# Kernel optimization log

Measured on AMD Instinct MI355X. Metric: run time of the kernel, lower is better.

The kernel has to match this reference:

```python
import jax, jax.numpy as jnp
import numpy as np

N_NODES = 50000
N_EDGES = 800000
D = 128


def _gcn_norm(edge_index, edge_weights, n_nodes):
    # PyG gcn_norm with add_self_loops=True, fill_value=1.0
    src = jnp.concatenate([edge_index[0], jnp.arange(n_nodes)])
    dst = jnp.concatenate([edge_index[1], jnp.arange(n_nodes)])
    w = jnp.concatenate([edge_weights, jnp.ones((n_nodes,), edge_weights.dtype)])
    deg = jax.ops.segment_sum(w, dst, num_segments=n_nodes)
    dinv = jnp.where(deg > 0, jax.lax.rsqrt(deg), 0.0)
    norm = dinv[src] * w * dinv[dst]  # [E + N]
    return src, dst, norm


def _gcn_conv(x, src, dst, norm, W, b, n_nodes):
    h = x @ W                                   # [N, F_out]
    msg = h[src] * norm[:, None]                # gather + scale, [E+N, F_out]
    out = jax.ops.segment_sum(msg, dst, num_segments=n_nodes)
    return out + b


def setup_inputs() -> dict:
    key = jax.random.key(0)
    ks = jax.random.split(key, 12)
    s = 1.0 / np.sqrt(D)
    return {
        "x": jax.random.normal(ks[0], (N_NODES, D), jnp.float32),
        "edge_index": jax.random.randint(ks[1], (2, N_EDGES), 0, N_NODES, jnp.int64),
        "edge_weights": jax.random.uniform(ks[2], (N_EDGES,), jnp.float32),
        "W1": jax.random.normal(ks[3], (D, D), jnp.float32) * s,
        "b1": jnp.zeros((D,), jnp.float32),
        "W2": jax.random.normal(ks[4], (D, D), jnp.float32) * s,
        "b2": jnp.zeros((D,), jnp.float32),
        "W3": jax.random.normal(ks[5], (D, D), jnp.float32) * s,
        "b3": jnp.zeros((D,), jnp.float32),
        "Wl": jax.random.normal(ks[6], (D, D), jnp.float32) * s,
        "bl": jnp.zeros((D,), jnp.float32),
    }


def reference(x, edge_index, edge_weights, W1, b1, W2, b2, W3, b3, Wl, bl):
    n = x.shape[0]
    src, dst, norm = _gcn_norm(edge_index, edge_weights, n)
    h = _gcn_conv(x, src, dst, norm, W1, b1, n)
    h = jax.nn.relu(h)
    h = _gcn_conv(h, src, dst, norm, W2, b2, n)
    h = jax.nn.relu(h)
    h = _gcn_conv(h, src, dst, norm, W3, b3, n)
    # final 'linear' activation entry == nn.Linear(out_size, out_size)
    return h @ Wl + bl
```

## Files before the change

kernel.cpp:

```cpp
#include <hip/hip_runtime.h>
#include <hip/hip_fp16.h>


#define D 128

typedef __attribute__((ext_vector_type(8))) _Float16 half8;
typedef __attribute__((ext_vector_type(4))) float floatx4;

#define CNT_STRIDE 16

__global__ __launch_bounds__(256) void k_edge_pass1(const int* __restrict__ dst,
                                                    unsigned int* __restrict__ cntp,
                                                    int* __restrict__ loc, int E) {
    int e = blockIdx.x * 256 + threadIdx.x;
    if (e < E) {
        int d = dst[e];
        loc[e] = (int)atomicAdd(&cntp[(size_t)d * CNT_STRIDE], 1u);
    }
}

__device__ inline int block_exscan_256(int v) {
    int tid = threadIdx.x;
    int lane = tid & 63, wv = tid >> 6;
    int incl = v;
#pragma unroll
    for (int d = 1; d < 64; d <<= 1) {
        int n = __shfl_up(incl, d, 64);
        if (lane >= d) incl += n;
    }
    __shared__ int wsum[4];
    if (lane == 63) wsum[wv] = incl;
    __syncthreads();
    int woff = 0;
#pragma unroll
    for (int j = 0; j < 4; j++) woff += (j < wv) ? wsum[j] : 0;
    return woff + incl - v;
}

__global__ __launch_bounds__(256) void k_scan_a(const unsigned int* __restrict__ cntp,
                                                int* bsum, int N) {
    int i = blockIdx.x * 256 + threadIdx.x;
    int v = (i < N) ? (int)cntp[(size_t)i * CNT_STRIDE] : 0;
#pragma unroll
    for (int d = 32; d; d >>= 1) v += __shfl_down(v, d, 64);
    __shared__ int ws4[4];
    int lane = threadIdx.x & 63, wv = threadIdx.x >> 6;
    if (lane == 0) ws4[wv] = v;
    __syncthreads();
    if (threadIdx.x == 0) bsum[blockIdx.x] = ws4[0] + ws4[1] + ws4[2] + ws4[3];
}

__global__ __launch_bounds__(256) void k_scan_b(const int* __restrict__ bsum,
                                                int* boff, int nb) {
    int tid = threadIdx.x;
    int v = (tid < nb) ? bsum[tid] : 0;
    int ex = block_exscan_256(v);
    if (tid < nb) boff[tid] = ex;
}

__global__ __launch_bounds__(256) void k_scan_c(const unsigned int* __restrict__ cntp,
                                                const int* __restrict__ boff,
                                                int* rp, int N, int E) {
    int i = blockIdx.x * 256 + threadIdx.x;
    int v = (i < N) ? (int)cntp[(size_t)i * CNT_STRIDE] : 0;
    int ex = block_exscan_256(v);
    if (i < N) rp[i] = boff[blockIdx.x] + ex;
    if (i == 0) rp[N] = E;
}

__global__ __launch_bounds__(256) void k_fill(const int* __restrict__ ei,
                                              const float* __restrict__ w,
                                              const int* __restrict__ rp,
                                              const int* __restrict__ loc,
                                              unsigned int* __restrict__ ev, int E) {
    int e = blockIdx.x * 256 + threadIdx.x;
    if (e < E) {
        int s = ei[e];
        int d = ei[E + e];
        int p = rp[d] + loc[e];
        unsigned int wq = (unsigned int)__float2uint_rn(w[e] * 32767.0f);
        ev[p] = (wq << 17) | (unsigned int)s;
    }
}

__global__ __launch_bounds__(256) void k_deg(const int* __restrict__ rp,
                                             const unsigned int* __restrict__ ev,
                                             float* __restrict__ dinv, int N) {
    int i = blockIdx.x * 256 + threadIdx.x;
    if (i < N) {
        int e0 = rp[i], e1 = rp[i + 1];
        float s = 0.f;
        for (int e = e0; e < e1; e++)
            s += (float)(ev[e] >> 17);
        dinv[i] = rsqrtf(1.0f + s * (1.0f / 32767.0f));
    }
}

template <bool A_IS_F32>
__global__ __launch_bounds__(256) void k_gemm_mfma(const void* __restrict__ Aptr,
                                                   const float* __restrict__ W,
                                                   const float* __restrict__ dinv,
                                                   const float* __restrict__ bias,
                                                   float* __restrict__ C32,
                                                   __half* __restrict__ C16, int N) {
    __shared__ _Float16 Wl[128][136];
    int tid = threadIdx.x;

#pragma unroll
    for (int j = 0; j < 64; j++) {
        int e = tid + j * 256;
        int k = e >> 7, n = e & 127;
        Wl[n][k] = (_Float16)W[e];
    }
    __syncthreads();

    int wave = tid >> 6, lane = tid & 63;
    int m = lane & 15, q = lane >> 4;
    int R0 = blockIdx.x * 128 + wave * 32;

    const float*  A32p = (const float*)Aptr;
    const __half* A16p = (const __half*)Aptr;

    floatx4 acc[2][8];
#pragma unroll
    for (int rt = 0; rt < 2; rt++)
#pragma unroll
        for (int ct = 0; ct < 8; ct++) acc[rt][ct] = (floatx4){0.f, 0.f, 0.f, 0.f};

#pragma unroll
    for (int kk = 0; kk < 4; kk++) {
        half8 a[2];
#pragma unroll
        for (int rt = 0; rt < 2; rt++) {
            int row = R0 + rt * 16 + m;
            half8 t = {0, 0, 0, 0, 0, 0, 0, 0};
            if (row < N) {
                if (A_IS_F32) {
                    const float* p = &A32p[(size_t)row * 128 + kk * 32 + q * 8];
                    float4 f0 = *(const float4*)p;
                    float4 f1 = *(const float4*)(p + 4);
                    t[0] = (_Float16)f0.x; t[1] = (_Float16)f0.y;
                    t[2] = (_Float16)f0.z; t[3] = (_Float16)f0.w;
                    t[4] = (_Float16)f1.x; t[5] = (_Float16)f1.y;
                    t[6] = (_Float16)f1.z; t[7] = (_Float16)f1.w;
                } else {
                    t = *(const half8*)&A16p[(size_t)row * 128 + kk * 32 + q * 8];
                }
            }
            a[rt] = t;
        }
#pragma unroll
        for (int ct = 0; ct < 8; ct++) {
            half8 b = *(const half8*)&Wl[ct * 16 + m][kk * 32 + q * 8];
            acc[0][ct] = __builtin_amdgcn_mfma_f32_16x16x32_f16(a[0], b, acc[0][ct], 0, 0, 0);
            acc[1][ct] = __builtin_amdgcn_mfma_f32_16x16x32_f16(a[1], b, acc[1][ct], 0, 0, 0);
        }
    }

#pragma unroll
    for (int rt = 0; rt < 2; rt++) {
#pragma unroll
        for (int r = 0; r < 4; r++) {
            int row = R0 + rt * 16 + q * 4 + r;
            if (row >= N) continue;
            float dv = (dinv != nullptr) ? dinv[row] : 1.0f;
#pragma unroll
            for (int ct = 0; ct < 8; ct++) {
                int col = ct * 16 + m;
                float v = acc[rt][ct][r] * dv;
                if (C16) C16[(size_t)row * 128 + col] = __float2half_rn(v);
                if (C32) C32[(size_t)row * 128 + col] = v + bias[col];
            }
        }
    }
}

__global__ __launch_bounds__(256) void k_agg(const __half* __restrict__ y16,
                                             const int* __restrict__ rp,
                                             const unsigned int* __restrict__ ev,
                                             const float* __restrict__ dinv,
                                             const float* __restrict__ bias,
                                             __half* __restrict__ out16,
                                             int N, int relu) {
    int wave = blockIdx.x * 4 + (threadIdx.x >> 6);
    if (wave >= N) return;
    int lane = threadIdx.x & 63;
    int g = lane >> 4;
    int sl = lane & 15;
    int i = wave;

    float acc[8];
#pragma unroll
    for (int j = 0; j < 8; j++) acc[j] = 0.f;

    int e0 = rp[i], e1 = rp[i + 1];
    int e = e0;

#define GFMA(Q, V)                                                        \
    {                                                                     \
        union { uint4 u; __half2 h2[4]; } U; U.u = (Q);                   \
        float2 f0 = __half22float2(U.h2[0]);                              \
        float2 f1 = __half22float2(U.h2[1]);                              \
        float2 f2 = __half22float2(U.h2[2]);                              \
        float2 f3 = __half22float2(U.h2[3]);                              \
        acc[0] = fmaf(V, f0.x, acc[0]); acc[1] = fmaf(V, f0.y, acc[1]);   \
        acc[2] = fmaf(V, f1.x, acc[2]); acc[3] = fmaf(V, f1.y, acc[3]);   \
        acc[4] = fmaf(V, f2.x, acc[4]); acc[5] = fmaf(V, f2.y, acc[5]);   \
        acc[6] = fmaf(V, f3.x, acc[6]); acc[7] = fmaf(V, f3.y, acc[7]);   \
    }
#define UNPK(P, C, V)                                                     \
    int   C = (int)((P) & 0x1FFFFu);                                      \
    float V = (float)((P) >> 17) * (1.0f / 32767.0f);

    for (; e + 16 <= e1; e += 16) {
        unsigned int pA = ev[e + g];
        unsigned int pB = ev[e + 4 + g];
        unsigned int pC = ev[e + 8 + g];
        unsigned int pD = ev[e + 12 + g];
        UNPK(pA, cA, vA); UNPK(pB, cB, vB); UNPK(pC, cC, vC); UNPK(pD, cD, vD);
        uint4 qA = *(const uint4*)&y16[(size_t)cA * D + sl * 8];
        uint4 qB = *(const uint4*)&y16[(size_t)cB * D + sl * 8];
        uint4 qC = *(const uint4*)&y16[(size_t)cC * D + sl * 8];
        uint4 qD = *(const uint4*)&y16[(size_t)cD * D + sl * 8];
        GFMA(qA, vA); GFMA(qB, vB); GFMA(qC, vC); GFMA(qD, vD);
    }
    if (e + 8 <= e1) {
        unsigned int pA = ev[e + g];
        unsigned int pB = ev[e + 4 + g];
        UNPK(pA, cA, vA); UNPK(pB, cB, vB);
        uint4 qA = *(const uint4*)&y16[(size_t)cA * D + sl * 8];
        uint4 qB = *(const uint4*)&y16[(size_t)cB * D + sl * 8];
        GFMA(qA, vA); GFMA(qB, vB);
        e += 8;
    }
    if (e + 4 <= e1) {
        unsigned int pA = ev[e + g];
        UNPK(pA, cA, vA);
        uint4 qA = *(const uint4*)&y16[(size_t)cA * D + sl * 8];
        GFMA(qA, vA);
        e += 4;
    }
    if (e + g < e1) {
        unsigned int pA = ev[e + g];
        UNPK(pA, cA, vA);
        uint4 qA = *(const uint4*)&y16[(size_t)cA * D + sl * 8];
        GFMA(qA, vA);
    }
#undef UNPK
#undef GFMA

#pragma unroll
    for (int j = 0; j < 8; j++) {
        acc[j] += __shfl_xor(acc[j], 16, 64);
        acc[j] += __shfl_xor(acc[j], 32, 64);
    }

    if (g == 0) {
        float di = dinv[i];
        union { uint4 u; __half2 h2[4]; } S;
        S.u = *(const uint4*)&y16[(size_t)i * D + sl * 8];
        float2 s0 = __half22float2(S.h2[0]);
        float2 s1 = __half22float2(S.h2[1]);
        float2 s2 = __half22float2(S.h2[2]);
        float2 s3 = __half22float2(S.h2[3]);
        float4 b0 = *(const float4*)&bias[sl * 8];
        float4 b1 = *(const float4*)&bias[sl * 8 + 4];
        float o[8];
        o[0] = b0.x + di * (acc[0] + s0.x);
        o[1] = b0.y + di * (acc[1] + s0.y);
        o[2] = b0.z + di * (acc[2] + s1.x);
        o[3] = b0.w + di * (acc[3] + s1.y);
        o[4] = b1.x + di * (acc[4] + s2.x);
        o[5] = b1.y + di * (acc[5] + s2.y);
        o[6] = b1.z + di * (acc[6] + s3.x);
        o[7] = b1.w + di * (acc[7] + s3.y);
        if (relu) {
#pragma unroll
            for (int j = 0; j < 8; j++) o[j] = fmaxf(o[j], 0.f);
        }
        union { uint4 u; __half2 h2[4]; } O;
        O.h2[0] = __float22half2_rn(make_float2(o[0], o[1]));
        O.h2[1] = __float22half2_rn(make_float2(o[2], o[3]));
        O.h2[2] = __float22half2_rn(make_float2(o[4], o[5]));
        O.h2[3] = __float22half2_rn(make_float2(o[6], o[7]));
        *(uint4*)&out16[(size_t)i * D + sl * 8] = O.u;
    }
}

extern "C" void kernel_launch(void* const* d_in, const int* in_sizes, int n_in,
                              void* d_out, int out_size, void* d_ws, size_t ws_size,
                              hipStream_t stream) {
    const float* x  = (const float*)d_in[0];
    const int*   ei = (const int*)d_in[1];
    const float* ew = (const float*)d_in[2];
    const float* W1 = (const float*)d_in[3];
    const float* b1 = (const float*)d_in[4];
    const float* W2 = (const float*)d_in[5];
    const float* b2 = (const float*)d_in[6];
    const float* W3 = (const float*)d_in[7];
    const float* b3 = (const float*)d_in[8];
    const float* Wl = (const float*)d_in[9];
    const float* bl = (const float*)d_in[10];

    int N = in_sizes[0] / D;
    int E = in_sizes[2];

    char* ws = (char*)d_ws;
    size_t off = 0;
    auto alloc = [&](size_t bytes) {
        void* p = ws + off;
        off = (off + bytes + 255) & ~(size_t)255;
        return p;
    };
    unsigned int* cntp = (unsigned int*)alloc((size_t)N * CNT_STRIDE * 4);
    float*  dinv = (float*)alloc((size_t)N * 4);
    int*    bsum = (int*)  alloc(1024);
    int*    boff = (int*)  alloc(1024);
    int*    rp   = (int*)  alloc((size_t)(N + 1) * 4);
    int*    loc  = (int*)  alloc((size_t)E * 4);
    unsigned int* ev = (unsigned int*)alloc((size_t)E * 4);
    __half* y16  = (__half*)alloc((size_t)N * D * 2);
    __half* z16  = (__half*)alloc((size_t)N * D * 2);

    int nbN = (N + 255) / 256;
    int nbE = (E + 255) / 256;

    hipMemsetAsync(cntp, 0, (size_t)N * CNT_STRIDE * 4, stream);
    k_edge_pass1<<<nbE, 256, 0, stream>>>(ei + E, cntp, loc, E);
    k_scan_a<<<nbN, 256, 0, stream>>>(cntp, bsum, N);
    k_scan_b<<<1, 256, 0, stream>>>(bsum, boff, nbN);
    k_scan_c<<<nbN, 256, 0, stream>>>(cntp, boff, rp, N, E);
    k_fill<<<nbE, 256, 0, stream>>>(ei, ew, rp, loc, ev, E);
    k_deg<<<nbN, 256, 0, stream>>>(rp, ev, dinv, N);

    int gg = (N + 127) / 128;
    int ga = (N + 3) / 4;

    k_gemm_mfma<true ><<<gg, 256, 0, stream>>>(x,   W1, dinv, nullptr, nullptr, y16, N);
    k_agg<<<ga, 256, 0, stream>>>(y16, rp, ev, dinv, b1, z16, N, 1);
    k_gemm_mfma<false><<<gg, 256, 0, stream>>>(z16, W2, dinv, nullptr, nullptr, y16, N);
    k_agg<<<ga, 256, 0, stream>>>(y16, rp, ev, dinv, b2, z16, N, 1);
    k_gemm_mfma<false><<<gg, 256, 0, stream>>>(z16, W3, dinv, nullptr, nullptr, y16, N);
    k_agg<<<ga, 256, 0, stream>>>(y16, rp, ev, dinv, b3, z16, N, 0);
    k_gemm_mfma<false><<<gg, 256, 0, stream>>>(z16, Wl, nullptr, bl, (float*)d_out, nullptr, N);
}
```

Baseline: 305.0 us.

## Split aggregation feature dimension into four slices across blocks

The aggregation kernel now assigns each node to four waves in four different blocks, each wave covering a 32-column slice of the 128 features. Within a wave, 8 lanes cover the slice with 4 halves each and 8 edge groups run in parallel, in place of 16 lanes of 8 halves and 4 edge groups. This raises wave count and edge-level parallelism, aiming to hide gather latency. In exchange it loads the edge list four times, issues narrower 8-byte gathers, and drops the deeper unrolled loop, so fewer loads are in flight per wave.

Result: slower. 448.3 us (+46.9%).

```diff
diff --git a/kernel.cpp b/kernel.cpp
--- a/kernel.cpp
+++ b/kernel.cpp
@@ -182,108 +182,67 @@
                                              const float* __restrict__ bias,
                                              __half* __restrict__ out16,
                                              int N, int relu) {
-    int wave = blockIdx.x * 4 + (threadIdx.x >> 6);
-    if (wave >= N) return;
+    int s = blockIdx.x & 3;
+    int i = (blockIdx.x >> 2) * 4 + (threadIdx.x >> 6);
+    if (i >= N) return;
     int lane = threadIdx.x & 63;
-    int g = lane >> 4;
-    int sl = lane & 15;
-    int i = wave;
-
-    float acc[8];
-#pragma unroll
-    for (int j = 0; j < 8; j++) acc[j] = 0.f;
+    int g = lane >> 3;
+    int sl = lane & 7;
+    int fo = s * 32 + sl * 4;
+
+    float a0 = 0.f, a1 = 0.f, a2 = 0.f, a3 = 0.f;
 
     int e0 = rp[i], e1 = rp[i + 1];
     int e = e0;
 
-#define GFMA(Q, V)                                                        \
+#define GFMA(P)                                                           \
     {                                                                     \
-        union { uint4 u; __half2 h2[4]; } U; U.u = (Q);                   \
+        int   c = (int)((P) & 0x1FFFFu);                                  \
+        float v = (float)((P) >> 17) * (1.0f / 32767.0f);                 \
+        union { uint2 u; __half2 h2[2]; } U;                              \
+        U.u = *(const uint2*)&y16[(size_t)c * D + fo];                    \
         float2 f0 = __half22float2(U.h2[0]);                              \
         float2 f1 = __half22float2(U.h2[1]);                              \
-        float2 f2 = __half22float2(U.h2[2]);                              \
-        float2 f3 = __half22float2(U.h2[3]);                              \
-        acc[0] = fmaf(V, f0.x, acc[0]); acc[1] = fmaf(V, f0.y, acc[1]);   \
-        acc[2] = fmaf(V, f1.x, acc[2]); acc[3] = fmaf(V, f1.y, acc[3]);   \
-        acc[4] = fmaf(V, f2.x, acc[4]); acc[5] = fmaf(V, f2.y, acc[5]);   \
-        acc[6] = fmaf(V, f3.x, acc[6]); acc[7] = fmaf(V, f3.y, acc[7]);   \
-    }
-#define UNPK(P, C, V)                                                     \
-    int   C = (int)((P) & 0x1FFFFu);                                      \
-    float V = (float)((P) >> 17) * (1.0f / 32767.0f);
-
-    for (; e + 16 <= e1; e += 16) {
-        unsigned int pA = ev[e + g];
-        unsigned int pB = ev[e + 4 + g];
-        unsigned int pC = ev[e + 8 + g];
-        unsigned int pD = ev[e + 12 + g];
-        UNPK(pA, cA, vA); UNPK(pB, cB, vB); UNPK(pC, cC, vC); UNPK(pD, cD, vD);
-        uint4 qA = *(const uint4*)&y16[(size_t)cA * D + sl * 8];
-        uint4 qB = *(const uint4*)&y16[(size_t)cB * D + sl * 8];
-        uint4 qC = *(const uint4*)&y16[(size_t)cC * D + sl * 8];
-        uint4 qD = *(const uint4*)&y16[(size_t)cD * D + sl * 8];
-        GFMA(qA, vA); GFMA(qB, vB); GFMA(qC, vC); GFMA(qD, vD);
-    }
-    if (e + 8 <= e1) {
-        unsigned int pA = ev[e + g];
-        unsigned int pB = ev[e + 4 + g];
-        UNPK(pA, cA, vA); UNPK(pB, cB, vB);
-        uint4 qA = *(const uint4*)&y16[(size_t)cA * D + sl * 8];
-        uint4 qB = *(const uint4*)&y16[(size_t)cB * D + sl * 8];
-        GFMA(qA, vA); GFMA(qB, vB);
-        e += 8;
-    }
-    if (e + 4 <= e1) {
-        unsigned int pA = ev[e + g];
-        UNPK(pA, cA, vA);
-        uint4 qA = *(const uint4*)&y16[(size_t)cA * D + sl * 8];
-        GFMA(qA, vA);
-        e += 4;
+        a0 = fmaf(v, f0.x, a0); a1 = fmaf(v, f0.y, a1);                   \
+        a2 = fmaf(v, f1.x, a2); a3 = fmaf(v, f1.y, a3);                   \
+    }
+
+    for (; e + 8 <= e1; e += 8) {
+        unsigned int p = ev[e + g];
+        GFMA(p);
     }
     if (e + g < e1) {
-        unsigned int pA = ev[e + g];
-        UNPK(pA, cA, vA);
-        uint4 qA = *(const uint4*)&y16[(size_t)cA * D + sl * 8];
-        GFMA(qA, vA);
-    }
-#undef UNPK
+        unsigned int p = ev[e + g];
+        GFMA(p);
+    }
 #undef GFMA
 
-#pragma unroll
-    for (int j = 0; j < 8; j++) {
-        acc[j] += __shfl_xor(acc[j], 16, 64);
-        acc[j] += __shfl_xor(acc[j], 32, 64);
-    }
+    a0 += __shfl_xor(a0, 8, 64);  a1 += __shfl_xor(a1, 8, 64);
+    a2 += __shfl_xor(a2, 8, 64);  a3 += __shfl_xor(a3, 8, 64);
+    a0 += __shfl_xor(a0, 16, 64); a1 += __shfl_xor(a1, 16, 64);
+    a2 += __shfl_xor(a2, 16, 64); a3 += __shfl_xor(a3, 16, 64);
+    a0 += __shfl_xor(a0, 32, 64); a1 += __shfl_xor(a1, 32, 64);
+    a2 += __shfl_xor(a2, 32, 64); a3 += __shfl_xor(a3, 32, 64);
 
     if (g == 0) {
         float di = dinv[i];
-        union { uint4 u; __half2 h2[4]; } S;
-        S.u = *(const uint4*)&y16[(size_t)i * D + sl * 8];
+        union { uint2 u; __half2 h2[2]; } S;
+        S.u = *(const uint2*)&y16[(size_t)i * D + fo];
         float2 s0 = __half22float2(S.h2[0]);
         float2 s1 = __half22float2(S.h2[1]);
-        float2 s2 = __half22float2(S.h2[2]);
-        float2 s3 = __half22float2(S.h2[3]);
-        float4 b0 = *(const float4*)&bias[sl * 8];
-        float4 b1 = *(const float4*)&bias[sl * 8 + 4];
-        float o[8];
-        o[0] = b0.x + di * (acc[0] + s0.x);
-        o[1] = b0.y + di * (acc[1] + s0.y);
-        o[2] = b0.z + di * (acc[2] + s1.x);
-        o[3] = b0.w + di * (acc[3] + s1.y);
-        o[4] = b1.x + di * (acc[4] + s2.x);
-        o[5] = b1.y + di * (acc[5] + s2.y);
-        o[6] = b1.z + di * (acc[6] + s3.x);
-        o[7] = b1.w + di * (acc[7] + s3.y);
+        float4 b = *(const float4*)&bias[fo];
+        float o0 = b.x + di * (a0 + s0.x);
+        float o1 = b.y + di * (a1 + s0.y);
+        float o2 = b.z + di * (a2 + s1.x);
+        float o3 = b.w + di * (a3 + s1.y);
         if (relu) {
-#pragma unroll
-            for (int j = 0; j < 8; j++) o[j] = fmaxf(o[j], 0.f);
+            o0 = fmaxf(o0, 0.f); o1 = fmaxf(o1, 0.f);
+            o2 = fmaxf(o2, 0.f); o3 = fmaxf(o3, 0.f);
         }
-        union { uint4 u; __half2 h2[4]; } O;
-        O.h2[0] = __float22half2_rn(make_float2(o[0], o[1]));
-        O.h2[1] = __float22half2_rn(make_float2(o[2], o[3]));
-        O.h2[2] = __float22half2_rn(make_float2(o[4], o[5]));
-        O.h2[3] = __float22half2_rn(make_float2(o[6], o[7]));
-        *(uint4*)&out16[(size_t)i * D + sl * 8] = O.u;
+        union { uint2 u; __half2 h2[2]; } O;
+        O.h2[0] = __float22half2_rn(make_float2(o0, o1));
+        O.h2[1] = __float22half2_rn(make_float2(o2, o3));
+        *(uint2*)&out16[(size_t)i * D + fo] = O.u;
     }
 }
 
@@ -334,7 +293,7 @@
     k_deg<<<nbN, 256, 0, stream>>>(rp, ev, dinv, N);
 
     int gg = (N + 127) / 128;
-    int ga = (N + 3) / 4;
+    int ga = ((N + 3) / 4) * 4;
 
     k_gemm_mfma<true ><<<gg, 256, 0, stream>>>(x,   W1, dinv, nullptr, nullptr, y16, N);
     k_agg<<<ga, 256, 0, stream>>>(y16, rp, ev, dinv, b1, z16, N, 1);
```
